# Kernel optimization log

Hardware: AMD Instinct MI355X
Metric: run time of the kernel (lower is better)

The kernel has to match this reference:

```python
import jax, jax.numpy as jnp
import numpy as np

EPS = 1e-5

def layer_norm(x, w, b):
    m = jnp.mean(x, axis=-1, keepdims=True)
    v = jnp.mean(jnp.square(x - m), axis=-1, keepdims=True)
    return (x - m) * jax.lax.rsqrt(v + EPS) * w + b

def setup_inputs() -> dict:
    key = jax.random.key(0)
    B, S, D, H = 4, 2048, 768, 12
    Dh, F = D // H, 4 * D
    ks = jax.random.split(key, 16)
    s = 0.02
    return {
        "x":    jax.random.normal(ks[0], (B, S, D), dtype=jnp.float32),
        # per-head q/k/v projections stacked over heads: [H, D, Dh]
        "Wq":   jax.random.normal(ks[1], (H, D, Dh), dtype=jnp.float32) * s,
        "bq":   jnp.zeros((H, Dh), dtype=jnp.float32),
        "Wk":   jax.random.normal(ks[2], (H, D, Dh), dtype=jnp.float32) * s,
        "bk":   jnp.zeros((H, Dh), dtype=jnp.float32),
        "Wv":   jax.random.normal(ks[3], (H, D, Dh), dtype=jnp.float32) * s,
        "bv":   jnp.zeros((H, Dh), dtype=jnp.float32),
        "Wo":   jax.random.normal(ks[4], (D, D), dtype=jnp.float32) * s,
        "bo":   jnp.zeros((D,), dtype=jnp.float32),
        "W1":   jax.random.normal(ks[5], (D, F), dtype=jnp.float32) * s,
        "b1":   jnp.zeros((F,), dtype=jnp.float32),
        "W2":   jax.random.normal(ks[6], (F, D), dtype=jnp.float32) * s,
        "b2":   jnp.zeros((D,), dtype=jnp.float32),
        "ln1_w": jnp.ones((D,), dtype=jnp.float32),
        "ln1_b": jnp.zeros((D,), dtype=jnp.float32),
        "ln2_w": jnp.ones((D,), dtype=jnp.float32),
        "ln2_b": jnp.zeros((D,), dtype=jnp.float32),
    }

def reference(x, Wq, bq, Wk, bk, Wv, bv, Wo, bo, W1, b1, W2, b2,
              ln1_w, ln1_b, ln2_w, ln2_b):
    B, S, D = x.shape
    H, _, Dh = Wq.shape
    scale = jnp.sqrt(jnp.float32(Dh))  # torch scales by sqrt(dout)
    # q,k,v: [B, H, S, Dh]
    q = jnp.einsum('bsd,hde->bhse', x, Wq) + bq[None, :, None, :]
    k = jnp.einsum('bsd,hde->bhse', x, Wk) + bk[None, :, None, :]
    v = jnp.einsum('bsd,hde->bhse', x, Wv) + bv[None, :, None, :]
    scores = jnp.einsum('bhqe,bhke->bhqk', q, k) / scale  # [B,H,S,S]
    causal = jnp.tril(jnp.ones((S, S), dtype=bool))
    scores = jnp.where(causal[None, None], scores, -jnp.inf)
    attn = jax.nn.softmax(scores, axis=-1)
    ctx = jnp.einsum('bhqk,bhke->bhqe', attn, v)           # [B,H,S,Dh]
    ctx = jnp.transpose(ctx, (0, 2, 1, 3)).reshape(B, S, D)  # concat heads
    att_out = ctx @ Wo + bo
    h = layer_norm(x + att_out, ln1_w, ln1_b)  # post-norm, dropout=0
    ff = jax.nn.gelu(h @ W1 + b1, approximate=False) @ W2 + b2
    return layer_norm(h + ff, ln2_w, ln2_b)
```

## Files before the change

### kernel.cpp

```cpp
#include <hip/hip_runtime.h>
#include <hip/hip_bf16.h>
#include <math.h>

#define B_ 4
#define S_ 2048
#define D_ 768
#define H_ 12
#define DH_ 64
#define F_ 3072
#define NTOK (B_*S_)
#define BH_ (B_*H_)

typedef __hip_bfloat16 bf16;
typedef __attribute__((ext_vector_type(8))) short bf16x8;
typedef __attribute__((ext_vector_type(4))) float f32x4;
typedef __attribute__((ext_vector_type(4))) _Float16 half4;
typedef __attribute__((ext_vector_type(8))) _Float16 half8;
typedef __attribute__((ext_vector_type(2))) __fp16 fp16x2;

#define GLD16(g, l) __builtin_amdgcn_global_load_lds( \
    (__attribute__((address_space(1))) void*)(uintptr_t)(g), \
    (__attribute__((address_space(3))) void*)(uintptr_t)(l), 16, 0, 0)

__device__ __forceinline__ float bs2f(short s){
  union { unsigned int u; float f; } cv; cv.u = ((unsigned int)(unsigned short)s) << 16; return cv.f;
}
__device__ __forceinline__ float b2f(bf16 v){ return __bfloat162float(v); }
__device__ __forceinline__ bf16 f2b(float v){ return __float2bfloat16(v); }
__device__ __forceinline__ short f2bb(float v){ bf16 b = f2b(v); short s; __builtin_memcpy(&s, &b, 2); return s; }

__device__ __forceinline__ half4 pk4(float p0, float p1, float p2, float p3){
  union { fp16x2 v2[2]; half4 v4; } u;
  u.v2[0] = __builtin_amdgcn_cvt_pkrtz(p0, p1);
  u.v2[1] = __builtin_amdgcn_cvt_pkrtz(p2, p3);
  return u.v4;
}

__device__ __forceinline__ void wgbar(){
  __builtin_amdgcn_s_barrier();
  asm volatile("" ::: "memory");
}
__device__ __forceinline__ void wgbar_lds(){
  asm volatile("s_waitcnt lgkmcnt(0)" ::: "memory");
  __builtin_amdgcn_s_barrier();
  asm volatile("" ::: "memory");
}

__device__ __forceinline__ float gelu_fast(float v){
  const float c0 = -2.302208157f;
  const float c1 = -0.102943238f;
  float w = v*v;
  float z = v * __builtin_fmaf(c1, w, c0);
  float t = __builtin_amdgcn_exp2f(z);
  return v * __builtin_amdgcn_rcpf(1.0f + t);
}

__global__ void f32_to_bf16_k(const float4* __restrict__ in, short4* __restrict__ out, int n4){
  int i = blockIdx.x*256 + threadIdx.x;
  if (i < n4){
    float4 v = in[i];
    short4 o;
    o.x = f2bb(v.x); o.y = f2bb(v.y); o.z = f2bb(v.z); o.w = f2bb(v.w);
    out[i] = o;
  }
}

__global__ __launch_bounds__(256) void transpose_f32_bf16_k(const float* __restrict__ in,
    bf16* __restrict__ out, int K, int N){
  __shared__ float t[32][33];
  const int kb = blockIdx.y*32, nb = blockIdx.x*32;
  const int x = threadIdx.x & 31, y = threadIdx.x >> 5;
#pragma unroll
  for (int yy = y; yy < 32; yy += 8)
    t[yy][x] = in[(size_t)(kb+yy)*N + nb + x];
  __syncthreads();
#pragma unroll
  for (int yy = y; yy < 32; yy += 8)
    out[(size_t)(nb+yy)*K + kb + x] = f2b(t[x][yy]);
}

__global__ void pack_qkv_t_k(const float* __restrict__ Wq, const float* __restrict__ bq,
                             const float* __restrict__ Wk, const float* __restrict__ bk,
                             const float* __restrict__ Wv, const float* __restrict__ bv,
                             bf16* __restrict__ Wt, float* __restrict__ bcat){
  int idx = blockIdx.x*256 + threadIdx.x;
  if (idx < 3*D_*D_){
    int n = idx / D_;
    int k = idx - n*D_;
    int which = n / D_;
    int cc = n - which*D_;
    int h = cc >> 6, e = cc & 63;
    const float* W = (which==0) ? Wq : ((which==1) ? Wk : Wv);
    Wt[idx] = f2b(W[((size_t)h*D_ + k)*DH_ + e]);
  }
  if (idx < 3*D_){
    int which = idx / D_;
    int cc = idx - which*D_;
    int h = cc >> 6, e = cc & 63;
    const float* bb = (which==0) ? bq : ((which==1) ? bk : bv);
    bcat[idx] = bb[h*DH_ + e];
  }
}

template<int EPI>
__global__ __launch_bounds__(256) void mgemm128_k(
    const bf16* __restrict__ A, const bf16* __restrict__ Bt,
    const float* __restrict__ bias, const bf16* __restrict__ aux,
    bf16* __restrict__ C, int M, int N, int K,
    bf16* __restrict__ qb, bf16* __restrict__ kbuf, _Float16* __restrict__ vt)
{
  __shared__ __align__(16) bf16 As[16384];
  __shared__ __align__(16) bf16 Bs[16384];
  const int tid  = threadIdx.x;
  const int wave = tid >> 6, lane = tid & 63;
  const int quad = lane >> 4, l16 = lane & 15;
  const int wm = (wave >> 1) * 64, wn = (wave & 1) * 64;

  const int NX = gridDim.x;
  const int f  = blockIdx.y * NX + blockIdx.x;
  const int xcd = f & 7;
  const int j   = f >> 3;
  const int bx  = j % NX;
  const int by  = (j / NX) * 8 + xcd;
  const int m0 = by * 128, n0 = bx * 128;

  const int srow8 = lane >> 3;
  const int g     = (lane & 7) ^ srow8;
  const bf16* gA = A  + (size_t)(m0 + wave*32 + srow8)*K + g*8;
  const bf16* gB = Bt + (size_t)(n0 + wave*32 + srow8)*K + g*8;
  const uintptr_t asb = (uintptr_t)(void*)As + (size_t)wave*32*128;
  const uintptr_t bsb = (uintptr_t)(void*)Bs + (size_t)wave*32*128;

  f32x4 acc[4][4];
#pragma unroll
  for (int i=0;i<4;i++)
#pragma unroll
    for (int j2=0;j2<4;j2++) acc[i][j2] = (f32x4)0.f;

  const char* AsB = (const char*)As;
  const char* BsB = (const char*)Bs;
  const int KT = K >> 6;

#pragma unroll
  for (int t=0;t<4;t++){
    GLD16(gA + (size_t)t*8*K, asb + t*1024);
    GLD16(gB + (size_t)t*8*K, bsb + t*1024);
  }
  gA += 64; gB += 64;
  asm volatile("s_waitcnt vmcnt(0)" ::: "memory");
  wgbar();

  for (int kt = 0; kt < KT; ++kt){
    const int cur = kt & 1, nxt = cur ^ 1;
    const bool pf = (kt + 1) < KT;
    if (pf){
      const uintptr_t ao = asb + (size_t)nxt*16384;
      const uintptr_t bo = bsb + (size_t)nxt*16384;
#pragma unroll
      for (int t=0;t<4;t++){
        GLD16(gA + (size_t)t*8*K, ao + t*1024);
        GLD16(gB + (size_t)t*8*K, bo + t*1024);
      }
      gA += 64; gB += 64;
    }
    const char* Ac = AsB + (size_t)cur*16384;
    const char* Bc = BsB + (size_t)cur*16384;
#pragma unroll
    for (int kq = 0; kq < 2; kq++){
      const int cbase = kq*4 + quad;
      bf16x8 af[4], bfr[4];
#pragma unroll
      for (int i=0;i<4;i++){
        const int m = wm + i*16 + l16;
        af[i] = *(const bf16x8*)(Ac + (m << 7) + ((cbase ^ (m & 7)) << 4));
      }
#pragma unroll
      for (int j2=0;j2<4;j2++){
        const int n = wn + j2*16 + l16;
        bfr[j2] = *(const bf16x8*)(Bc + (n << 7) + ((cbase ^ (n & 7)) << 4));
      }
#pragma unroll
      for (int i=0;i<4;i++)
#pragma unroll
        for (int j2=0;j2<4;j2++)
          acc[i][j2] = __builtin_amdgcn_mfma_f32_16x16x32_bf16(af[i], bfr[j2], acc[i][j2], 0, 0, 0);
    }
    if (pf) asm volatile("s_waitcnt vmcnt(0)" ::: "memory");
    wgbar();
  }

#pragma unroll
  for (int i=0;i<4;i++){
#pragma unroll
    for (int j2=0;j2<4;j2++){
      const int n = n0 + wn + j2*16 + l16;
      const int m_base = m0 + wm + i*16 + quad*4;
      if (EPI == 0){
        const int which = n / D_;
        const int cc = n - which*D_;
        const int h = cc >> 6, e = cc & 63;
        if (which == 2){
          const int b = m_base >> 11, s = m_base & (S_-1);
          const int sl = s & 63;
          const int perm = ((sl>>2)&3)*16 + ((sl>>4)&3)*4;
          half4 hv;
#pragma unroll
          for (int r=0;r<4;r++) hv[r] = (_Float16)(acc[i][j2][r] + bias[n]);
          *(half4*)(vt + ((size_t)(b*H_+h)*DH_ + e)*S_ + (s & ~63) + perm) = hv;
        } else {
          bf16* dst = (which==0) ? qb : kbuf;
          const float sc2 = (which==0) ? 0.18033688f : 1.0f;
#pragma unroll
          for (int r=0;r<4;r++){
            const int m = m_base + r;
            const int b = m >> 11, s = m & (S_-1);
            dst[((size_t)(b*H_+h)*S_ + s)*DH_ + e] = f2b((acc[i][j2][r] + bias[n]) * sc2);
          }
        }
      } else if (EPI == 1){
#pragma unroll
        for (int r=0;r<4;r++){
          const int m = m_base + r;
          float v = acc[i][j2][r] + bias[n] + b2f(aux[(size_t)m*N + n]);
          C[(size_t)m*N + n] = f2b(v);
        }
      } else {
#pragma unroll
        for (int r=0;r<4;r++){
          const int m = m_base + r;
          float v = acc[i][j2][r] + bias[n];
          C[(size_t)m*N + n] = f2b(gelu_fast(v));
        }
      }
    }
  }
}

__global__ __launch_bounds__(256, 4) void fattn_k(const bf16* __restrict__ qb,
    const bf16* __restrict__ kb, const _Float16* __restrict__ vt, bf16* __restrict__ ctx)
{
  __shared__ __align__(16) char smem[38400];
  typedef bf16     KsRow[72];
  typedef _Float16 VsRow[72];
  KsRow* kp0 = (KsRow*)(smem);
  KsRow* kp1 = (KsRow*)(smem + 9216);
  VsRow* vp0 = (VsRow*)(smem + 18432);
  VsRow* vp1 = (VsRow*)(smem + 27648);
  float* maxb  = (float*)(smem + 36864);
  float* libuf = (float*)(smem + 37888);
  float* Obuf  = (float*)smem;

  const int bh = blockIdx.x;
  const int qt = 31 - blockIdx.y;
  const int q0 = qt * 64;
  const int tid = threadIdx.x;
  const int wave = tid >> 6, lane = tid & 63;
  const int quad = lane >> 4, l16 = lane & 15;
  const int kh = wave >> 1, qh = wave & 1;
  const size_t kbase = (size_t)bh * S_ * DH_;
  const int nt = qt + 1;

  const int sr  = tid >> 2;
  const int seg = (tid & 3) * 16;

  bf16x8 qf[2][2];
#pragma unroll
  for (int nf=0; nf<2; nf++)
#pragma unroll
    for (int h=0; h<2; h++)
      qf[nf][h] = *(const bf16x8*)(qb + kbase + (size_t)(q0 + qh*32 + nf*16 + l16)*DH_ + h*32 + quad*8);

  f32x4 o[4][2];
#pragma unroll
  for (int df=0; df<4; df++){ o[df][0] = (f32x4)0.f; o[df][1] = (f32x4)0.f; }
  float mi[2] = {-1e30f, -1e30f}, li[2] = {0.f, 0.f};

  bf16x8 ka0, ka1; half8 va0, va1;
  {
    const bf16* ks = kb + kbase + (size_t)sr*DH_ + seg;
    ka0 = *(const bf16x8*)ks; ka1 = *(const bf16x8*)(ks + 8);
    const _Float16* vs = vt + ((size_t)bh*DH_ + sr)*S_ + seg;
    va0 = *(const half8*)vs; va1 = *(const half8*)(vs + 8);
  }
  *(bf16x8*)&kp0[sr][seg]   = ka0;
  *(bf16x8*)&kp0[sr][seg+8] = ka1;
  *(half8*)&vp0[sr][seg]    = va0;
  *(half8*)&vp0[sr][seg+8]  = va1;
  if (nt > 1){
    const bf16* ks = kb + kbase + (size_t)(64 + sr)*DH_ + seg;
    ka0 = *(const bf16x8*)ks; ka1 = *(const bf16x8*)(ks + 8);
    const _Float16* vs = vt + ((size_t)bh*DH_ + sr)*S_ + 64 + seg;
    va0 = *(const half8*)vs; va1 = *(const half8*)(vs + 8);
  }
  wgbar_lds();

  for (int kt = 0; kt < nt; ++kt){
    bf16x8 af[2][2];
#pragma unroll
    for (int mf=0; mf<2; mf++)
#pragma unroll
      for (int h=0; h<2; h++)
        af[mf][h] = *(const bf16x8*)&kp0[kh*32 + mf*16 + l16][h*32 + quad*8];
    f32x4 sc[2][2];
#pragma unroll
    for (int mf=0; mf<2; mf++)
#pragma unroll
      for (int nf=0; nf<2; nf++){
        f32x4 t = __builtin_amdgcn_mfma_f32_16x16x32_bf16(af[mf][0], qf[nf][0], (f32x4)0.f, 0, 0, 0);
        sc[mf][nf] = __builtin_amdgcn_mfma_f32_16x16x32_bf16(af[mf][1], qf[nf][1], t, 0, 0, 0);
      }

    if (kt == qt){
#pragma unroll
      for (int mf=0; mf<2; mf++){
        const int keyl = kh*32 + mf*16 + quad*4;
#pragma unroll
        for (int nf=0; nf<2; nf++){
          const int ql = qh*32 + nf*16 + l16;
#pragma unroll
          for (int r=0; r<4; r++)
            if (keyl + r > ql) sc[mf][nf][r] = -1e30f;
        }
      }
    }

    float mw[2];
#pragma unroll
    for (int nf=0; nf<2; nf++){
      float mx = -1e30f;
#pragma unroll
      for (int mf=0; mf<2; mf++)
#pragma unroll
        for (int r=0; r<4; r++) mx = fmaxf(mx, sc[mf][nf][r]);
      mx = fmaxf(mx, __shfl_xor(mx, 16));
      mx = fmaxf(mx, __shfl_xor(mx, 32));
      mw[nf] = mx;
    }
    float* mb = maxb + (kt & 1)*128;
    if (quad == 0){
      mb[kh*64 + qh*32 + l16]      = mw[0];
      mb[kh*64 + qh*32 + 16 + l16] = mw[1];
    }

    half8 vv[4];
#pragma unroll
    for (int df=0; df<4; df++)
      vv[df] = *(const half8*)&vp0[df*16 + l16][quad*16 + kh*8];

    if (kt + 1 < nt){
      *(bf16x8*)&kp1[sr][seg]   = ka0;
      *(bf16x8*)&kp1[sr][seg+8] = ka1;
      *(half8*)&vp1[sr][seg]    = va0;
      *(half8*)&vp1[sr][seg+8]  = va1;
      if (kt + 2 < nt){
        const int k0n = (kt + 2) * 64;
        const bf16* ks = kb + kbase + (size_t)(k0n + sr)*DH_ + seg;
        ka0 = *(const bf16x8*)ks; ka1 = *(const bf16x8*)(ks + 8);
        const _Float16* vs = vt + ((size_t)bh*DH_ + sr)*S_ + k0n + seg;
        va0 = *(const half8*)vs; va1 = *(const half8*)(vs + 8);
      }
    }
    wgbar_lds();

    const float tm0 = fmaxf(mw[0], mb[(1-kh)*64 + qh*32 + l16]);
    const float tm1 = fmaxf(mw[1], mb[(1-kh)*64 + qh*32 + 16 + l16]);
    const bool need = !__all((tm0 - mi[0] <= 8.f) && (tm1 - mi[1] <= 8.f));
    if (need){
      const float mn0 = fmaxf(mi[0], tm0);
      const float mn1 = fmaxf(mi[1], tm1);
      const float a0 = __builtin_amdgcn_exp2f(mi[0] - mn0);
      const float a1 = __builtin_amdgcn_exp2f(mi[1] - mn1);
      mi[0] = mn0; mi[1] = mn1;
      li[0] *= a0; li[1] *= a1;
#pragma unroll
      for (int df=0; df<4; df++)
#pragma unroll
        for (int r=0; r<4; r++){ o[df][0][r] *= a0; o[df][1][r] *= a1; }
    }

    half4 pfr[2][2];
#pragma unroll
    for (int nf=0; nf<2; nf++){
      float rs = 0.f;
#pragma unroll
      for (int mf=0; mf<2; mf++){
        const float p0 = __builtin_amdgcn_exp2f(sc[mf][nf][0] - mi[nf]);
        const float p1 = __builtin_amdgcn_exp2f(sc[mf][nf][1] - mi[nf]);
        const float p2 = __builtin_amdgcn_exp2f(sc[mf][nf][2] - mi[nf]);
        const float p3 = __builtin_amdgcn_exp2f(sc[mf][nf][3] - mi[nf]);
        rs += (p0 + p1) + (p2 + p3);
        pfr[mf][nf] = pk4(p0, p1, p2, p3);
      }
      rs += __shfl_xor(rs, 16);
      rs += __shfl_xor(rs, 32);
      li[nf] += rs;
    }

#pragma unroll
    for (int df=0; df<4; df++){
      half4 vlo = __builtin_shufflevector(vv[df], vv[df], 0,1,2,3);
      half4 vhi = __builtin_shufflevector(vv[df], vv[df], 4,5,6,7);
#pragma unroll
      for (int nf=0; nf<2; nf++){
        o[df][nf] = __builtin_amdgcn_mfma_f32_16x16x16f16(vlo, pfr[0][nf], o[df][nf], 0, 0, 0);
        o[df][nf] = __builtin_amdgcn_mfma_f32_16x16x16f16(vhi, pfr[1][nf], o[df][nf], 0, 0, 0);
      }
    }

    { KsRow* t_ = kp0; kp0 = kp1; kp1 = t_; }
    { VsRow* t_ = vp0; vp0 = vp1; vp1 = t_; }
  }

  __syncthreads();
  if (quad == 0){
    libuf[kh*64 + qh*32 + l16]      = li[0];
    libuf[kh*64 + qh*32 + 16 + l16] = li[1];
  }
  if (kh == 1){
#pragma unroll
    for (int df=0; df<4; df++)
#pragma unroll
      for (int nf=0; nf<2; nf++)
#pragma unroll
        for (int r=0; r<4; r++)
          Obuf[(qh*64 + df*16 + quad*4 + r)*33 + nf*16 + l16] = o[df][nf][r];
  }
  __syncthreads();
  if (kh == 0){
    const int b = bh / H_, h = bh - (bh / H_)*H_;
#pragma unroll
    for (int nf=0; nf<2; nf++){
      const int q64 = qh*32 + nf*16 + l16;
      const float inv = 1.0f / (libuf[q64] + libuf[64 + q64]);
      const int qtok = q0 + q64;
#pragma unroll
      for (int df=0; df<4; df++){
        short4 pk;
        float v0 = (o[df][nf][0] + Obuf[(qh*64 + df*16 + quad*4 + 0)*33 + nf*16 + l16]) * inv;
        float v1 = (o[df][nf][1] + Obuf[(qh*64 + df*16 + quad*4 + 1)*33 + nf*16 + l16]) * inv;
        float v2 = (o[df][nf][2] + Obuf[(qh*64 + df*16 + quad*4 + 2)*33 + nf*16 + l16]) * inv;
        float v3 = (o[df][nf][3] + Obuf[(qh*64 + df*16 + quad*4 + 3)*33 + nf*16 + l16]) * inv;
        pk.x = f2bb(v0); pk.y = f2bb(v1); pk.z = f2bb(v2); pk.w = f2bb(v3);
        *(short4*)((short*)ctx + ((size_t)(b*S_ + qtok))*D_ + h*DH_ + df*16 + quad*4) = pk;
      }
    }
  }
}

template<typename T> __device__ __forceinline__ void st4(T* p, size_t idx, float a, float b, float c, float d);
template<> __device__ __forceinline__ void st4<float>(float* p, size_t idx, float a, float b, float c, float d){
  float4 v; v.x=a; v.y=b; v.z=c; v.w=d; *(float4*)(p+idx) = v;
}
template<> __device__ __forceinline__ void st4<bf16>(bf16* p, size_t idx, float a, float b, float c, float d){
  short4 v; v.x=f2bb(a); v.y=f2bb(b); v.z=f2bb(c); v.w=f2bb(d); *(short4*)((short*)p+idx) = v;
}

template<typename OutT>
__global__ __launch_bounds__(192) void layernorm_k(const bf16* __restrict__ X,
    const float* __restrict__ g, const float* __restrict__ bta, OutT* __restrict__ Y)
{
  const int row = blockIdx.x;
  const int tid = threadIdx.x;
  const short4 raw = *(const short4*)((const short*)X + (size_t)row*D_ + tid*4);
  const float v0 = bs2f(raw.x), v1 = bs2f(raw.y), v2 = bs2f(raw.z), v3 = bs2f(raw.w);
  float s  = v0+v1+v2+v3;
  float s2 = v0*v0+v1*v1+v2*v2+v3*v3;
#pragma unroll
  for (int o = 32; o > 0; o >>= 1){ s += __shfl_down(s, o); s2 += __shfl_down(s2, o); }
  __shared__ float rs[3], rq[3];
  const int lane = tid & 63, w = tid >> 6;
  if (lane == 0){ rs[w] = s; rq[w] = s2; }
  __syncthreads();
  s  = rs[0]+rs[1]+rs[2];
  s2 = rq[0]+rq[1]+rq[2];
  const float mean = s * (1.0f/D_);
  const float var  = s2 * (1.0f/D_) - mean*mean;
  const float inv  = rsqrtf(var + 1e-5f);
  const float4 g4 = *(const float4*)(g + tid*4);
  const float4 b4 = *(const float4*)(bta + tid*4);
  st4(Y, (size_t)row*D_ + tid*4,
      (v0-mean)*inv*g4.x + b4.x,
      (v1-mean)*inv*g4.y + b4.y,
      (v2-mean)*inv*g4.z + b4.z,
      (v3-mean)*inv*g4.w + b4.w);
}

extern "C" void kernel_launch(void* const* d_in, const int* in_sizes, int n_in,
                              void* d_out, int out_size, void* d_ws, size_t ws_size,
                              hipStream_t stream)
{
  const float* x   = (const float*)d_in[0];
  const float* Wq  = (const float*)d_in[1];
  const float* bq  = (const float*)d_in[2];
  const float* Wk  = (const float*)d_in[3];
  const float* bk  = (const float*)d_in[4];
  const float* Wv  = (const float*)d_in[5];
  const float* bv  = (const float*)d_in[6];
  const float* Wo  = (const float*)d_in[7];
  const float* bo  = (const float*)d_in[8];
  const float* W1  = (const float*)d_in[9];
  const float* b1  = (const float*)d_in[10];
  const float* W2  = (const float*)d_in[11];
  const float* b2  = (const float*)d_in[12];
  const float* g1  = (const float*)d_in[13];
  const float* be1 = (const float*)d_in[14];
  const float* g2  = (const float*)d_in[15];
  const float* be2 = (const float*)d_in[16];
  float* out = (float*)d_out;

  char* ws = (char*)d_ws;
  size_t off = 0;
  auto alloc = [&](size_t bytes)->char*{
    char* p = ws + off; off = (off + bytes + 255) & ~(size_t)255; return p;
  };
  bf16*  xb    = (bf16*) alloc((size_t)NTOK*D_*2);
  bf16*  WcatT = (bf16*) alloc((size_t)3*D_*D_*2);
  float* bcat  = (float*)alloc((size_t)3*D_*4);
  bf16*  WoT   = (bf16*) alloc((size_t)D_*D_*2);
  bf16*  W1T   = (bf16*) alloc((size_t)F_*D_*2);
  bf16*  W2T   = (bf16*) alloc((size_t)D_*F_*2);
  bf16*  r1    = (bf16*) alloc((size_t)NTOK*F_*2);
  bf16*  qb    = r1;
  bf16*  kb    = r1 + (size_t)NTOK*D_;
  _Float16* vt = (_Float16*)(r1 + (size_t)2*NTOK*D_);
  bf16*  ff1   = r1;
  bf16*  ctxb  = (bf16*) alloc((size_t)NTOK*D_*2);
  bf16*  y1    = (bf16*) alloc((size_t)NTOK*D_*2);
  bf16*  hb    = (bf16*) alloc((size_t)NTOK*D_*2);
  bf16*  y2    = ctxb;

  f32_to_bf16_k<<<(NTOK*D_/4+255)/256, 256, 0, stream>>>(
      (const float4*)x, (short4*)xb, NTOK*D_/4);
  transpose_f32_bf16_k<<<dim3(D_/32, D_/32), 256, 0, stream>>>(Wo, WoT, D_, D_);
  transpose_f32_bf16_k<<<dim3(F_/32, D_/32), 256, 0, stream>>>(W1, W1T, D_, F_);
  transpose_f32_bf16_k<<<dim3(D_/32, F_/32), 256, 0, stream>>>(W2, W2T, F_, D_);
  pack_qkv_t_k<<<(3*D_*D_+255)/256, 256, 0, stream>>>(Wq,bq,Wk,bk,Wv,bv,WcatT,bcat);

  mgemm128_k<0><<<dim3(3*D_/128, NTOK/128), 256, 0, stream>>>(
      xb, WcatT, bcat, nullptr, nullptr, NTOK, 3*D_, D_, qb, kb, vt);

  fattn_k<<<dim3(BH_, S_/64), 256, 0, stream>>>(qb, kb, vt, ctxb);

  mgemm128_k<1><<<dim3(D_/128, NTOK/128), 256, 0, stream>>>(
      ctxb, WoT, bo, xb, y1, NTOK, D_, D_, nullptr, nullptr, nullptr);

  layernorm_k<bf16><<<NTOK, 192, 0, stream>>>(y1, g1, be1, hb);

  mgemm128_k<2><<<dim3(F_/128, NTOK/128), 256, 0, stream>>>(
      hb, W1T, b1, nullptr, ff1, NTOK, F_, D_, nullptr, nullptr, nullptr);

  mgemm128_k<1><<<dim3(D_/128, NTOK/128), 256, 0, stream>>>(
      ff1, W2T, b2, hb, y2, NTOK, D_, F_, nullptr, nullptr, nullptr);

  layernorm_k<float><<<NTOK, 192, 0, stream>>>(y2, g2, be2, out);
}
```

Before: 375.8 us.

## Give each attention wave its own 16 queries and merge prep kernels into one

```diff
diff --git a/kernel.cpp b/kernel.cpp
--- a/kernel.cpp
+++ b/kernel.cpp
@@ -55,51 +55,63 @@
   return v * __builtin_amdgcn_rcpf(1.0f + t);
 }
 
-__global__ void f32_to_bf16_k(const float4* __restrict__ in, short4* __restrict__ out, int n4){
-  int i = blockIdx.x*256 + threadIdx.x;
-  if (i < n4){
-    float4 v = in[i];
+__global__ __launch_bounds__(256) void prep_k(
+    const float4* __restrict__ x4, short4* __restrict__ xb4,
+    const float* __restrict__ Wo, bf16* __restrict__ WoT,
+    const float* __restrict__ W1, bf16* __restrict__ W1T,
+    const float* __restrict__ W2, bf16* __restrict__ W2T,
+    const float* __restrict__ Wq, const float* __restrict__ bq,
+    const float* __restrict__ Wk, const float* __restrict__ bk,
+    const float* __restrict__ Wv, const float* __restrict__ bv,
+    bf16* __restrict__ Wt, float* __restrict__ bcat)
+{
+  __shared__ float t[32][33];
+  int bid = blockIdx.x;
+  const int tidx = threadIdx.x;
+
+  if (bid < 6144){
+    const int i = bid*256 + tidx;
+    float4 v = x4[i];
     short4 o;
     o.x = f2bb(v.x); o.y = f2bb(v.y); o.z = f2bb(v.z); o.w = f2bb(v.w);
-    out[i] = o;
-  }
-}
-
-__global__ __launch_bounds__(256) void transpose_f32_bf16_k(const float* __restrict__ in,
-    bf16* __restrict__ out, int K, int N){
-  __shared__ float t[32][33];
-  const int kb = blockIdx.y*32, nb = blockIdx.x*32;
-  const int x = threadIdx.x & 31, y = threadIdx.x >> 5;
+    xb4[i] = o;
+    return;
+  }
+  bid -= 6144;
+  if (bid >= 576 + 2304 + 2304){
+    bid -= 576 + 2304 + 2304;
+    const int idx = bid*256 + tidx;
+    {
+      int n = idx / D_;
+      int k = idx - n*D_;
+      int which = n / D_;
+      int cc = n - which*D_;
+      int h = cc >> 6, e = cc & 63;
+      const float* W = (which==0) ? Wq : ((which==1) ? Wk : Wv);
+      Wt[idx] = f2b(W[((size_t)h*D_ + k)*DH_ + e]);
+    }
+    if (idx < 3*D_){
+      int which = idx / D_;
+      int cc = idx - which*D_;
+      int h = cc >> 6, e = cc & 63;
+      const float* bb = (which==0) ? bq : ((which==1) ? bk : bv);
+      bcat[idx] = bb[h*DH_ + e];
+    }
+    return;
+  }
+  const float* tin; bf16* tout; int K, N, tiles_x;
+  if (bid < 576){ tin = Wo; tout = WoT; K = D_; N = D_; tiles_x = 24; }
+  else if (bid < 576 + 2304){ bid -= 576; tin = W1; tout = W1T; K = D_; N = F_; tiles_x = 96; }
+  else { bid -= 576 + 2304; tin = W2; tout = W2T; K = F_; N = D_; tiles_x = 24; }
+  const int kb = (bid / tiles_x)*32, nb = (bid % tiles_x)*32;
+  const int xx = tidx & 31, y = tidx >> 5;
 #pragma unroll
   for (int yy = y; yy < 32; yy += 8)
-    t[yy][x] = in[(size_t)(kb+yy)*N + nb + x];
+    t[yy][xx] = tin[(size_t)(kb+yy)*N + nb + xx];
   __syncthreads();
 #pragma unroll
   for (int yy = y; yy < 32; yy += 8)
-    out[(size_t)(nb+yy)*K + kb + x] = f2b(t[x][yy]);
-}
-
-__global__ void pack_qkv_t_k(const float* __restrict__ Wq, const float* __restrict__ bq,
-                             const float* __restrict__ Wk, const float* __restrict__ bk,
-                             const float* __restrict__ Wv, const float* __restrict__ bv,
-                             bf16* __restrict__ Wt, float* __restrict__ bcat){
-  int idx = blockIdx.x*256 + threadIdx.x;
-  if (idx < 3*D_*D_){
-    int n = idx / D_;
-    int k = idx - n*D_;
-    int which = n / D_;
-    int cc = n - which*D_;
-    int h = cc >> 6, e = cc & 63;
-    const float* W = (which==0) ? Wq : ((which==1) ? Wk : Wv);
-    Wt[idx] = f2b(W[((size_t)h*D_ + k)*DH_ + e]);
-  }
-  if (idx < 3*D_){
-    int which = idx / D_;
-    int cc = idx - which*D_;
-    int h = cc >> 6, e = cc & 63;
-    const float* bb = (which==0) ? bq : ((which==1) ? bk : bv);
-    bcat[idx] = bb[h*DH_ + e];
-  }
+    tout[(size_t)(nb+yy)*K + kb + xx] = f2b(t[xx][yy]);
 }
 
 template<int EPI>
@@ -239,16 +251,13 @@
 __global__ __launch_bounds__(256, 4) void fattn_k(const bf16* __restrict__ qb,
     const bf16* __restrict__ kb, const _Float16* __restrict__ vt, bf16* __restrict__ ctx)
 {
-  __shared__ __align__(16) char smem[38400];
+  __shared__ __align__(16) char smem[36864];
   typedef bf16     KsRow[72];
   typedef _Float16 VsRow[72];
   KsRow* kp0 = (KsRow*)(smem);
   KsRow* kp1 = (KsRow*)(smem + 9216);
   VsRow* vp0 = (VsRow*)(smem + 18432);
   VsRow* vp1 = (VsRow*)(smem + 27648);
-  float* maxb  = (float*)(smem + 36864);
-  float* libuf = (float*)(smem + 37888);
-  float* Obuf  = (float*)smem;
 
   const int bh = blockIdx.x;
   const int qt = 31 - blockIdx.y;
@@ -256,24 +265,22 @@
   const int tid = threadIdx.x;
   const int wave = tid >> 6, lane = tid & 63;
   const int quad = lane >> 4, l16 = lane & 15;
-  const int kh = wave >> 1, qh = wave & 1;
   const size_t kbase = (size_t)bh * S_ * DH_;
   const int nt = qt + 1;
 
   const int sr  = tid >> 2;
   const int seg = (tid & 3) * 16;
 
-  bf16x8 qf[2][2];
-#pragma unroll
-  for (int nf=0; nf<2; nf++)
-#pragma unroll
-    for (int h=0; h<2; h++)
-      qf[nf][h] = *(const bf16x8*)(qb + kbase + (size_t)(q0 + qh*32 + nf*16 + l16)*DH_ + h*32 + quad*8);
-
-  f32x4 o[4][2];
-#pragma unroll
-  for (int df=0; df<4; df++){ o[df][0] = (f32x4)0.f; o[df][1] = (f32x4)0.f; }
-  float mi[2] = {-1e30f, -1e30f}, li[2] = {0.f, 0.f};
+  const int qloc = wave*16 + l16;
+  bf16x8 qf[2];
+#pragma unroll
+  for (int h=0; h<2; h++)
+    qf[h] = *(const bf16x8*)(qb + kbase + (size_t)(q0 + qloc)*DH_ + h*32 + quad*8);
+
+  f32x4 o[4];
+#pragma unroll
+  for (int df=0; df<4; df++) o[df] = (f32x4)0.f;
+  float mi = -1e30f, li = 0.f;
 
   bf16x8 ka0, ka1; half8 va0, va1;
   {
@@ -295,57 +302,39 @@
   wgbar_lds();
 
   for (int kt = 0; kt < nt; ++kt){
-    bf16x8 af[2][2];
-#pragma unroll
-    for (int mf=0; mf<2; mf++)
-#pragma unroll
-      for (int h=0; h<2; h++)
-        af[mf][h] = *(const bf16x8*)&kp0[kh*32 + mf*16 + l16][h*32 + quad*8];
-    f32x4 sc[2][2];
-#pragma unroll
-    for (int mf=0; mf<2; mf++)
-#pragma unroll
-      for (int nf=0; nf<2; nf++){
-        f32x4 t = __builtin_amdgcn_mfma_f32_16x16x32_bf16(af[mf][0], qf[nf][0], (f32x4)0.f, 0, 0, 0);
-        sc[mf][nf] = __builtin_amdgcn_mfma_f32_16x16x32_bf16(af[mf][1], qf[nf][1], t, 0, 0, 0);
+    f32x4 sc[4];
+#pragma unroll
+    for (int mf=0; mf<4; mf++){
+      bf16x8 a0 = *(const bf16x8*)&kp0[mf*16 + l16][quad*8];
+      bf16x8 a1 = *(const bf16x8*)&kp0[mf*16 + l16][32 + quad*8];
+      f32x4 t = __builtin_amdgcn_mfma_f32_16x16x32_bf16(a0, qf[0], (f32x4)0.f, 0, 0, 0);
+      sc[mf]  = __builtin_amdgcn_mfma_f32_16x16x32_bf16(a1, qf[1], t, 0, 0, 0);
+    }
+
+    if (kt == qt){
+#pragma unroll
+      for (int mf=0; mf<4; mf++){
+        const int keyl = mf*16 + quad*4;
+#pragma unroll
+        for (int r=0; r<4; r++)
+          if (keyl + r > qloc) sc[mf][r] = -1e30f;
       }
-
-    if (kt == qt){
-#pragma unroll
-      for (int mf=0; mf<2; mf++){
-        const int keyl = kh*32 + mf*16 + quad*4;
-#pragma unroll
-        for (int nf=0; nf<2; nf++){
-          const int ql = qh*32 + nf*16 + l16;
-#pragma unroll
-          for (int r=0; r<4; r++)
-            if (keyl + r > ql) sc[mf][nf][r] = -1e30f;
-        }
-      }
-    }
-
-    float mw[2];
-#pragma unroll
-    for (int nf=0; nf<2; nf++){
-      float mx = -1e30f;
-#pragma unroll
-      for (int mf=0; mf<2; mf++)
-#pragma unroll
-        for (int r=0; r<4; r++) mx = fmaxf(mx, sc[mf][nf][r]);
-      mx = fmaxf(mx, __shfl_xor(mx, 16));
-      mx = fmaxf(mx, __shfl_xor(mx, 32));
-      mw[nf] = mx;
-    }
-    float* mb = maxb + (kt & 1)*128;
-    if (quad == 0){
-      mb[kh*64 + qh*32 + l16]      = mw[0];
-      mb[kh*64 + qh*32 + 16 + l16] = mw[1];
-    }
-
-    half8 vv[4];
-#pragma unroll
-    for (int df=0; df<4; df++)
-      vv[df] = *(const half8*)&vp0[df*16 + l16][quad*16 + kh*8];
+    }
+
+    float mx = -1e30f;
+#pragma unroll
+    for (int mf=0; mf<4; mf++)
+#pragma unroll
+      for (int r=0; r<4; r++) mx = fmaxf(mx, sc[mf][r]);
+    mx = fmaxf(mx, __shfl_xor(mx, 16));
+    mx = fmaxf(mx, __shfl_xor(mx, 32));
+
+    half8 vva[4], vvb[4];
+#pragma unroll
+    for (int df=0; df<4; df++){
+      vva[df] = *(const half8*)&vp0[df*16 + l16][quad*16];
+      vvb[df] = *(const half8*)&vp0[df*16 + l16][quad*16 + 8];
+    }
 
     if (kt + 1 < nt){
       *(bf16x8*)&kp1[sr][seg]   = ka0;
@@ -362,88 +351,60 @@
     }
     wgbar_lds();
 
-    const float tm0 = fmaxf(mw[0], mb[(1-kh)*64 + qh*32 + l16]);
-    const float tm1 = fmaxf(mw[1], mb[(1-kh)*64 + qh*32 + 16 + l16]);
-    const bool need = !__all((tm0 - mi[0] <= 8.f) && (tm1 - mi[1] <= 8.f));
+    const bool need = !__all(mx - mi <= 8.f);
     if (need){
-      const float mn0 = fmaxf(mi[0], tm0);
-      const float mn1 = fmaxf(mi[1], tm1);
-      const float a0 = __builtin_amdgcn_exp2f(mi[0] - mn0);
-      const float a1 = __builtin_amdgcn_exp2f(mi[1] - mn1);
-      mi[0] = mn0; mi[1] = mn1;
-      li[0] *= a0; li[1] *= a1;
+      const float mn = fmaxf(mi, mx);
+      const float a = __builtin_amdgcn_exp2f(mi - mn);
+      mi = mn; li *= a;
 #pragma unroll
       for (int df=0; df<4; df++)
 #pragma unroll
-        for (int r=0; r<4; r++){ o[df][0][r] *= a0; o[df][1][r] *= a1; }
-    }
-
-    half4 pfr[2][2];
-#pragma unroll
-    for (int nf=0; nf<2; nf++){
-      float rs = 0.f;
-#pragma unroll
-      for (int mf=0; mf<2; mf++){
-        const float p0 = __builtin_amdgcn_exp2f(sc[mf][nf][0] - mi[nf]);
-        const float p1 = __builtin_amdgcn_exp2f(sc[mf][nf][1] - mi[nf]);
-        const float p2 = __builtin_amdgcn_exp2f(sc[mf][nf][2] - mi[nf]);
-        const float p3 = __builtin_amdgcn_exp2f(sc[mf][nf][3] - mi[nf]);
-        rs += (p0 + p1) + (p2 + p3);
-        pfr[mf][nf] = pk4(p0, p1, p2, p3);
-      }
-      rs += __shfl_xor(rs, 16);
-      rs += __shfl_xor(rs, 32);
-      li[nf] += rs;
-    }
+        for (int r=0; r<4; r++) o[df][r] *= a;
+    }
+
+    half4 pfr[4];
+    float rs = 0.f;
+#pragma unroll
+    for (int mf=0; mf<4; mf++){
+      const float p0 = __builtin_amdgcn_exp2f(sc[mf][0] - mi);
+      const float p1 = __builtin_amdgcn_exp2f(sc[mf][1] - mi);
+      const float p2 = __builtin_amdgcn_exp2f(sc[mf][2] - mi);
+      const float p3 = __builtin_amdgcn_exp2f(sc[mf][3] - mi);
+      rs += (p0 + p1) + (p2 + p3);
+      pfr[mf] = pk4(p0, p1, p2, p3);
+    }
+    rs += __shfl_xor(rs, 16);
+    rs += __shfl_xor(rs, 32);
+    li += rs;
 
 #pragma unroll
     for (int df=0; df<4; df++){
-      half4 vlo = __builtin_shufflevector(vv[df], vv[df], 0,1,2,3);
-      half4 vhi = __builtin_shufflevector(vv[df], vv[df], 4,5,6,7);
-#pragma unroll
-      for (int nf=0; nf<2; nf++){
-        o[df][nf] = __builtin_amdgcn_mfma_f32_16x16x16f16(vlo, pfr[0][nf], o[df][nf], 0, 0, 0);
-        o[df][nf] = __builtin_amdgcn_mfma_f32_16x16x16f16(vhi, pfr[1][nf], o[df][nf], 0, 0, 0);
-      }
+      half4 k0f = __builtin_shufflevector(vva[df], vva[df], 0,1,2,3);
+      half4 k1f = __builtin_shufflevector(vva[df], vva[df], 4,5,6,7);
+      half4 k2f = __builtin_shufflevector(vvb[df], vvb[df], 0,1,2,3);
+      half4 k3f = __builtin_shufflevector(vvb[df], vvb[df], 4,5,6,7);
+      o[df] = __builtin_amdgcn_mfma_f32_16x16x16f16(k0f, pfr[0], o[df], 0, 0, 0);
+      o[df] = __builtin_amdgcn_mfma_f32_16x16x16f16(k1f, pfr[1], o[df], 0, 0, 0);
+      o[df] = __builtin_amdgcn_mfma_f32_16x16x16f16(k2f, pfr[2], o[df], 0, 0, 0);
+      o[df] = __builtin_amdgcn_mfma_f32_16x16x16f16(k3f, pfr[3], o[df], 0, 0, 0);
     }
 
     { KsRow* t_ = kp0; kp0 = kp1; kp1 = t_; }
     { VsRow* t_ = vp0; vp0 = vp1; vp1 = t_; }
   }
 
-  __syncthreads();
-  if (quad == 0){
-    libuf[kh*64 + qh*32 + l16]      = li[0];
-    libuf[kh*64 + qh*32 + 16 + l16] = li[1];
-  }
-  if (kh == 1){
-#pragma unroll
-    for (int df=0; df<4; df++)
-#pragma unroll
-      for (int nf=0; nf<2; nf++)
-#pragma unroll
-        for (int r=0; r<4; r++)
-          Obuf[(qh*64 + df*16 + quad*4 + r)*33 + nf*16 + l16] = o[df][nf][r];
-  }
-  __syncthreads();
-  if (kh == 0){
-    const int b = bh / H_, h = bh - (bh / H_)*H_;
-#pragma unroll
-    for (int nf=0; nf<2; nf++){
-      const int q64 = qh*32 + nf*16 + l16;
-      const float inv = 1.0f / (libuf[q64] + libuf[64 + q64]);
-      const int qtok = q0 + q64;
-#pragma unroll
-      for (int df=0; df<4; df++){
-        short4 pk;
-        float v0 = (o[df][nf][0] + Obuf[(qh*64 + df*16 + quad*4 + 0)*33 + nf*16 + l16]) * inv;
-        float v1 = (o[df][nf][1] + Obuf[(qh*64 + df*16 + quad*4 + 1)*33 + nf*16 + l16]) * inv;
-        float v2 = (o[df][nf][2] + Obuf[(qh*64 + df*16 + quad*4 + 2)*33 + nf*16 + l16]) * inv;
-        float v3 = (o[df][nf][3] + Obuf[(qh*64 + df*16 + quad*4 + 3)*33 + nf*16 + l16]) * inv;
-        pk.x = f2bb(v0); pk.y = f2bb(v1); pk.z = f2bb(v2); pk.w = f2bb(v3);
-        *(short4*)((short*)ctx + ((size_t)(b*S_ + qtok))*D_ + h*DH_ + df*16 + quad*4) = pk;
-      }
-    }
+  const int b = bh / H_, h = bh - (bh / H_)*H_;
+  const float inv = 1.0f / li;
+  const int token = q0 + qloc;
+  short* cdst = (short*)ctx + ((size_t)(b*S_ + token))*D_ + h*DH_;
+#pragma unroll
+  for (int df=0; df<4; df++){
+    short4 pk;
+    pk.x = f2bb(o[df][0] * inv);
+    pk.y = f2bb(o[df][1] * inv);
+    pk.z = f2bb(o[df][2] * inv);
+    pk.w = f2bb(o[df][3] * inv);
+    *(short4*)(cdst + df*16 + quad*4) = pk;
   }
 }
 
@@ -529,12 +490,9 @@
   bf16*  hb    = (bf16*) alloc((size_t)NTOK*D_*2);
   bf16*  y2    = ctxb;
 
-  f32_to_bf16_k<<<(NTOK*D_/4+255)/256, 256, 0, stream>>>(
-      (const float4*)x, (short4*)xb, NTOK*D_/4);
-  transpose_f32_bf16_k<<<dim3(D_/32, D_/32), 256, 0, stream>>>(Wo, WoT, D_, D_);
-  transpose_f32_bf16_k<<<dim3(F_/32, D_/32), 256, 0, stream>>>(W1, W1T, D_, F_);
-  transpose_f32_bf16_k<<<dim3(D_/32, F_/32), 256, 0, stream>>>(W2, W2T, F_, D_);
-  pack_qkv_t_k<<<(3*D_*D_+255)/256, 256, 0, stream>>>(Wq,bq,Wk,bk,Wv,bv,WcatT,bcat);
+  prep_k<<<18240, 256, 0, stream>>>(
+      (const float4*)x, (short4*)xb, Wo, WoT, W1, W1T, W2, W2T,
+      Wq, bq, Wk, bk, Wv, bv, WcatT, bcat);
 
   mgemm128_k<0><<<dim3(3*D_/128, NTOK/128), 256, 0, stream>>>(
       xb, WcatT, bcat, nullptr, nullptr, NTOK, 3*D_, D_, qb, kb, vt);
```

Result: faster. 341.7 us (-9.1%).
